# Optimization experiments

Measured on AMD Instinct MI355X. Metric: run time of the kernel, lower is better.

## Reference

```python
import jax, jax.numpy as jnp
import numpy as np

N_EMBED = 1024
HEAD_SIZE = 64
SEQ_LEN = 4096
BATCH = 4


def setup_inputs() -> dict:
    key = jax.random.key(0)
    ks = jax.random.split(key, 7)
    scale = 1.0 / np.sqrt(N_EMBED)
    return {
        "x": jax.random.normal(ks[0], (BATCH, SEQ_LEN, N_EMBED), dtype=jnp.float32),
        "Wq": jax.random.normal(ks[1], (N_EMBED, HEAD_SIZE), dtype=jnp.float32) * scale,
        "bq": jax.random.normal(ks[2], (HEAD_SIZE,), dtype=jnp.float32) * 0.01,
        "Wk": jax.random.normal(ks[3], (N_EMBED, HEAD_SIZE), dtype=jnp.float32) * scale,
        "bk": jax.random.normal(ks[4], (HEAD_SIZE,), dtype=jnp.float32) * 0.01,
        "Wv": jax.random.normal(ks[5], (N_EMBED, HEAD_SIZE), dtype=jnp.float32) * scale,
        "bv": jax.random.normal(ks[6], (HEAD_SIZE,), dtype=jnp.float32) * 0.01,
    }


def reference(x, Wq, bq, Wk, bk, Wv, bv):
    # q, k, v: [B, S, H]
    q = x @ Wq + bq
    k = x @ Wk + bk
    v = x @ Wv + bv
    # raw scores [B, S, S]; original masks to -inf THEN divides by sqrt(head_size)
    # (-inf / sqrt = -inf, so equivalent to scaling finite entries only)
    scores = jnp.einsum("bqh,bkh->bqk", q, k)
    seq_len = x.shape[1]
    causal = jnp.tril(jnp.ones((seq_len, seq_len), dtype=bool))
    inv_scale = 1.0 / jnp.sqrt(jnp.asarray(HEAD_SIZE, dtype=scores.dtype))
    scores = jnp.where(causal, scores * inv_scale, -jnp.inf)
    weight = jax.nn.softmax(scores, axis=-1)
    # dropout is identity in eval / p=0
    out = jnp.einsum("bqk,bkh->bqh", weight, v)
    return out
```

## Files before the change

kernel.cpp:

```cpp
#include <hip/hip_runtime.h>
#include <hip/hip_bf16.h>

#define SS 4096
#define NROW 16384

typedef __attribute__((ext_vector_type(8))) short short8;
typedef __attribute__((ext_vector_type(4))) float f32x4;
typedef _Float16 half4 __attribute__((ext_vector_type(4)));

#define AS1 __attribute__((address_space(1)))
#define AS3 __attribute__((address_space(3)))

static __device__ __forceinline__ void glds16(const void* g, void* l) {
    __builtin_amdgcn_global_load_lds((const AS1 unsigned*)g, (AS3 unsigned*)l, 16, 0, 0);
}
static __device__ __forceinline__ short f2bf(float f) {
    union { float f; unsigned u; } v; v.f = f;
    unsigned r = v.u + 0x7FFFu + ((v.u >> 16) & 1u);
    return (short)(r >> 16);
}
static __device__ __forceinline__ unsigned pkbf(float lo, float hi) {
    union { float f; unsigned u; } x, y; x.f = lo; y.f = hi;
    return __builtin_amdgcn_perm(y.u + 0x8000u, x.u + 0x8000u, 0x07060302);
}
static __device__ __forceinline__ float bf2f(short s) {
    union { unsigned u; float f; } v;
    v.u = ((unsigned)(unsigned short)s) << 16;
    return v.f;
}

__global__ __launch_bounds__(256) void pack_w(const float* __restrict__ Wq,
                                              const float* __restrict__ Wk,
                                              const float* __restrict__ Wv,
                                              short* __restrict__ Wpack) {
    __shared__ float T[64 * 65];
    int bid = blockIdx.x;
    int nb = bid >> 4, kb = bid & 15;
    const float* W = (nb == 0) ? Wq : (nb == 1 ? Wk : Wv);
    int n0 = nb * 64, k0 = kb * 64;
    int tid = threadIdx.x;
    for (int ps = 0; ps < 16; ++ps) {
        int idx = tid + ps * 256;
        int kk = idx >> 6, nn = idx & 63;
        T[kk * 65 + nn] = W[(k0 + kk) * 64 + nn];
    }
    __syncthreads();
    for (int ps = 0; ps < 16; ++ps) {
        int idx = tid + ps * 256;
        int nn = idx >> 6, kk = idx & 63;
        Wpack[(n0 + nn) * 1024 + k0 + kk] = f2bf(T[kk * 65 + nn]);
    }
}

__global__ __launch_bounds__(256, 2) void proj_qkv(const float* __restrict__ x,
                                                   const short* __restrict__ Wpack,
                                                   const float* __restrict__ bq,
                                                   const float* __restrict__ bk,
                                                   const float* __restrict__ bv,
                                                   short* __restrict__ Qg,
                                                   short* __restrict__ Kg,
                                                   short* __restrict__ Vt) {
    __shared__ float Xs[2][32 * 64];
    __shared__ short Wsm[2][192 * 64];
    int tid = threadIdx.x, lane = tid & 63, wv = tid >> 6;
    int g = lane >> 4, c = lane & 15;
    int mh = wv & 1, nh = wv >> 1;
    int rowbase = blockIdx.x * 32;

    f32x4 acc[6];
    for (int i = 0; i < 6; ++i) acc[i] = (f32x4)(0.f);

    int xs0 = (wv * 2 + 0) * 64 + lane, xs1 = (wv * 2 + 1) * 64 + lane;
    int xr0 = xs0 >> 4, xp0 = (xs0 & 15) ^ (xr0 & 15);
    int xr1 = xs1 >> 4, xp1 = (xs1 & 15) ^ (xr1 & 15);

#define PROJ_ISSUE(nbs, k0)                                                              \
    do {                                                                                 \
        glds16(x + (rowbase + xr0) * 1024 + (k0) + xp0 * 4, &Xs[nbs][(wv * 2 + 0) * 256]); \
        glds16(x + (rowbase + xr1) * 1024 + (k0) + xp1 * 4, &Xs[nbs][(wv * 2 + 1) * 256]); \
        for (int j = 0; j < 6; ++j) {                                                    \
            int ws = (wv * 6 + j) * 64 + lane;                                           \
            int wr = ws >> 3, wp = (ws & 7) ^ (wr & 7);                                  \
            glds16(Wpack + wr * 1024 + (k0) + wp * 8, &Wsm[nbs][(wv * 6 + j) * 512]);    \
        }                                                                                \
    } while (0)

    PROJ_ISSUE(0, 0);

    for (int ko = 0; ko < 16; ++ko) {
        int bs = ko & 1;
        __syncthreads();
        if (ko < 15) PROJ_ISSUE(bs ^ 1, (ko + 1) * 64);
        for (int kc = 0; kc < 2; ++kc) {
            int h0 = kc * 8 + g * 2;
            float4 xa = *reinterpret_cast<const float4*>(&Xs[bs][(mh * 16 + c) * 64 + ((h0) ^ c) * 4]);
            float4 xb = *reinterpret_cast<const float4*>(&Xs[bs][(mh * 16 + c) * 64 + ((h0 + 1) ^ c) * 4]);
            short8 a;
            unsigned* aw = (unsigned*)&a;
            aw[0] = pkbf(xa.x, xa.y); aw[1] = pkbf(xa.z, xa.w);
            aw[2] = pkbf(xb.x, xb.y); aw[3] = pkbf(xb.z, xb.w);
            for (int nt = 0; nt < 6; ++nt) {
                int wrow = nh * 96 + nt * 16 + c;
                short8 b = *reinterpret_cast<const short8*>(&Wsm[bs][wrow * 64 + ((g + 4 * kc) ^ (c & 7)) * 8]);
                acc[nt] = __builtin_amdgcn_mfma_f32_16x16x32_bf16(a, b, acc[nt], 0, 0, 0);
            }
        }
    }
#undef PROJ_ISSUE

    const float SCQ = 0.125f * 1.4426950408889634f;
    _Float16* Vh = (_Float16*)Vt;
    for (int nt = 0; nt < 6; ++nt) {
        int col = nh * 96 + nt * 16 + c;
        for (int r = 0; r < 4; ++r) {
            int grow = rowbase + mh * 16 + g * 4 + r;
            float vv = acc[nt][r];
            if (col < 64) {
                Qg[grow * 64 + col] = f2bf((vv + bq[col]) * SCQ);
            } else if (col < 128) {
                Kg[grow * 64 + (col - 64)] = f2bf(vv + bk[col - 64]);
            } else {
                int f = col - 128;
                int batch = grow >> 12, s = grow & 4095;
                int key = s & 63;
                Vh[batch * 262144 + (s >> 6) * 4096 + f * 64 + (key ^ ((f & 15) * 4))] =
                    (_Float16)(vv + bv[f]);
            }
        }
    }
}

__global__ __launch_bounds__(256, 4) void attn(const short* __restrict__ Qg,
                                               const short* __restrict__ Kg,
                                               const short* __restrict__ Vt,
                                               short* __restrict__ Opart,
                                               float* __restrict__ Ls) {
    __shared__ short Kbuf[2][64 * 64];
    __shared__ short Vbuf[2][64 * 64];
    int tid = threadIdx.x, lane = tid & 63, wv = tid >> 6;
    int g = lane >> 4, c = lane & 15;

    int rb = 1151 - blockIdx.x;
    int batch = rb / 288;
    int j = rb - batch * 288;
    int gq = (int)((sqrtf((float)j + 1.0f) - 1.0f) * 0.5f);
    while (4 * (gq + 1) * (gq + 2) <= j) ++gq;
    while (4 * gq * (gq + 1) > j) --gq;
    int rem = j - 4 * gq * (gq + 1);
    int pidx = rem / (gq + 1);
    int ch = rem - pidx * (gq + 1);
    int p = gq * 8 + pidx;

    int t0 = ch * 8, t1 = min(t0 + 8, p + 1);
    int qrow0 = batch * SS + p * 64;
    const short* Kb = Kg + batch * SS * 64;
    const short* Vb = Vt + batch * SS * 64;

    short8 aq0 = *reinterpret_cast<const short8*>(Qg + (qrow0 + wv * 16 + c) * 64 + g * 8);
    short8 aq1 = *reinterpret_cast<const short8*>(Qg + (qrow0 + wv * 16 + c) * 64 + 32 + g * 8);

    f32x4 acc_o[4];
    for (int f = 0; f < 4; ++f) acc_o[f] = (f32x4)(0.f);
    float rs = 0.f;

    int s0 = wv * 128 + lane, s1 = s0 + 64;
    int r0 = s0 >> 3, q0 = (s0 & 7) ^ (r0 & 7);
    int r1 = s1 >> 3, q1 = (s1 & 7) ^ (r1 & 7);

#define ATTN_ISSUE(nbs, t)                                                  \
    do {                                                                    \
        glds16(Kb + (t) * 4096 + r0 * 64 + q0 * 8, &Kbuf[nbs][s0 * 8]);     \
        glds16(Kb + (t) * 4096 + r1 * 64 + q1 * 8, &Kbuf[nbs][s1 * 8]);     \
        glds16(Vb + (t) * 4096 + s0 * 8, &Vbuf[nbs][s0 * 8]);               \
        glds16(Vb + (t) * 4096 + s1 * 8, &Vbuf[nbs][s1 * 8]);               \
    } while (0)

    ATTN_ISSUE(0, t0);

    for (int t = t0; t < t1; ++t) {
        int bs = (t - t0) & 1;
        __syncthreads();
        if (t + 1 < t1) ATTN_ISSUE(bs ^ 1, t + 1);

        f32x4 s[4];
#pragma unroll
        for (int nt = 0; nt < 4; ++nt) {
            short8 k0 = *reinterpret_cast<const short8*>(&Kbuf[bs][(nt * 16 + c) * 64 + ((g) ^ (c & 7)) * 8]);
            short8 k1 = *reinterpret_cast<const short8*>(&Kbuf[bs][(nt * 16 + c) * 64 + ((g + 4) ^ (c & 7)) * 8]);
            s[nt] = (f32x4)(0.f);
            s[nt] = __builtin_amdgcn_mfma_f32_16x16x32_bf16(k0, aq0, s[nt], 0, 0, 0);
            s[nt] = __builtin_amdgcn_mfma_f32_16x16x32_bf16(k1, aq1, s[nt], 0, 0, 0);
        }

        half4 pb[4];
        if (t == p) {
#pragma unroll
            for (int nt = 0; nt < 4; ++nt)
                for (int r = 0; r < 4; ++r) {
                    int key = nt * 16 + g * 4 + r;
                    int row = wv * 16 + c;
                    float pv = (key <= row) ? __builtin_amdgcn_exp2f(s[nt][r]) : 0.f;
                    rs += pv;
                    pb[nt][r] = (_Float16)pv;
                }
        } else {
#pragma unroll
            for (int nt = 0; nt < 4; ++nt)
                for (int r = 0; r < 4; ++r) {
                    float pv = __builtin_amdgcn_exp2f(s[nt][r]);
                    rs += pv;
                    pb[nt][r] = (_Float16)pv;
                }
        }

#pragma unroll
        for (int nt = 0; nt < 4; ++nt) {
#pragma unroll
            for (int ft = 0; ft < 4; ++ft) {
                half4 va = *reinterpret_cast<const half4*>(
                    &Vbuf[bs][(ft * 16 + c) * 64 + ((nt * 16 + g * 4) ^ (c * 4))]);
                acc_o[ft] = __builtin_amdgcn_mfma_f32_16x16x16f16(va, pb[nt], acc_o[ft], 0, 0, 0);
            }
        }
    }
#undef ATTN_ISSUE

    float l = rs;
    l += __shfl_xor(l, 16);
    l += __shfl_xor(l, 32);
    float inv = 1.0f / l;

    int slot = ((batch * 64 + p) << 3) + ch;
    short* op = Opart + slot * 4096;
    int row = wv * 16 + c;
#pragma unroll
    for (int ft = 0; ft < 4; ++ft) {
        short4 ov;
        ov.x = f2bf(acc_o[ft][0] * inv);
        ov.y = f2bf(acc_o[ft][1] * inv);
        ov.z = f2bf(acc_o[ft][2] * inv);
        ov.w = f2bf(acc_o[ft][3] * inv);
        *reinterpret_cast<short4*>(op + row * 64 + ft * 16 + g * 4) = ov;
    }
    if (g == 0)
        Ls[slot * 64 + wv * 16 + c] = l;
}

__global__ __launch_bounds__(256) void merge_k(const short* __restrict__ Opart,
                                               const float* __restrict__ Ls,
                                               float* __restrict__ out) {
    int bP = blockIdx.x;
    int P = bP & 63, batch = bP >> 6;
    int nch = (P + 8) >> 3;
    int tid = threadIdx.x;
    int row = tid & 63, fg = tid >> 6;
    int slot0 = bP << 3;

    float w[8];
    float wsum = 0.f;
    for (int i = 0; i < nch; ++i) { w[i] = Ls[(slot0 + i) * 64 + row]; wsum += w[i]; }
    float invw = 1.0f / wsum;

    float o[16];
    for (int jj = 0; jj < 16; ++jj) o[jj] = 0.f;
    for (int i = 0; i < nch; ++i) {
        const short* op = Opart + (slot0 + i) * 4096 + row * 64 + fg * 16;
        short8 v0 = *reinterpret_cast<const short8*>(op);
        short8 v1 = *reinterpret_cast<const short8*>(op + 8);
        for (int jj = 0; jj < 8; ++jj) {
            o[jj]     += w[i] * bf2f(v0[jj]);
            o[8 + jj] += w[i] * bf2f(v1[jj]);
        }
    }
    int orow = batch * SS + P * 64 + row;
    for (int jj = 0; jj < 16; jj += 4) {
        float4 v;
        v.x = o[jj] * invw; v.y = o[jj + 1] * invw; v.z = o[jj + 2] * invw; v.w = o[jj + 3] * invw;
        *reinterpret_cast<float4*>(out + orow * 64 + fg * 16 + jj) = v;
    }
}

extern "C" void kernel_launch(void* const* d_in, const int* in_sizes, int n_in,
                              void* d_out, int out_size, void* d_ws, size_t ws_size,
                              hipStream_t stream) {
    const float* x  = (const float*)d_in[0];
    const float* Wq = (const float*)d_in[1];
    const float* bq = (const float*)d_in[2];
    const float* Wk = (const float*)d_in[3];
    const float* bk = (const float*)d_in[4];
    const float* Wv = (const float*)d_in[5];
    const float* bv = (const float*)d_in[6];
    float* out = (float*)d_out;

    short* Wpack = (short*)d_ws;
    short* Qg    = Wpack + 196608;
    short* Kg    = Qg + NROW * 64;
    short* Vt    = Kg + NROW * 64;
    short* Opart = Vt + NROW * 64;
    float* Ls    = (float*)(Opart + 2048 * 4096);

    hipLaunchKernelGGL(pack_w,   dim3(48),   dim3(256), 0, stream, Wq, Wk, Wv, Wpack);
    hipLaunchKernelGGL(proj_qkv, dim3(512),  dim3(256), 0, stream, x, Wpack, bq, bk, bv, Qg, Kg, Vt);
    hipLaunchKernelGGL(attn,     dim3(1152), dim3(256), 0, stream, Qg, Kg, Vt, Opart, Ls);
    hipLaunchKernelGGL(merge_k,  dim3(256),  dim3(256), 0, stream, Opart, Ls, out);
}
```

Baseline: 152.1 us.

## Shrink projection tiles to 16 rows and K=32 for more blocks in flight

The QKV projection kernel now has each block handle 16 rows instead of 32 and stages 32-wide K chunks instead of 64. The grid doubles to 1024 blocks and launch bounds allow 4 blocks per CU, with smaller LDS buffers and accumulators and reworked swizzles for the new tile shapes. The goal is better occupancy and more parallelism in this memory-bound pass over x. In exchange, the W tile is reloaded twice as often per row and there are twice as many barrier iterations.

```diff
diff --git a/kernel.cpp b/kernel.cpp
--- a/kernel.cpp
+++ b/kernel.cpp
@@ -52,7 +52,7 @@
     }
 }
 
-__global__ __launch_bounds__(256, 2) void proj_qkv(const float* __restrict__ x,
+__global__ __launch_bounds__(256, 4) void proj_qkv(const float* __restrict__ x,
                                                    const short* __restrict__ Wpack,
                                                    const float* __restrict__ bq,
                                                    const float* __restrict__ bk,
@@ -60,60 +60,57 @@
                                                    short* __restrict__ Qg,
                                                    short* __restrict__ Kg,
                                                    short* __restrict__ Vt) {
-    __shared__ float Xs[2][32 * 64];
-    __shared__ short Wsm[2][192 * 64];
+    __shared__ float Xs[2][16 * 32];
+    __shared__ short Wsm[2][192 * 32];
     int tid = threadIdx.x, lane = tid & 63, wv = tid >> 6;
     int g = lane >> 4, c = lane & 15;
-    int mh = wv & 1, nh = wv >> 1;
-    int rowbase = blockIdx.x * 32;
-
-    f32x4 acc[6];
-    for (int i = 0; i < 6; ++i) acc[i] = (f32x4)(0.f);
-
-    int xs0 = (wv * 2 + 0) * 64 + lane, xs1 = (wv * 2 + 1) * 64 + lane;
-    int xr0 = xs0 >> 4, xp0 = (xs0 & 15) ^ (xr0 & 15);
-    int xr1 = xs1 >> 4, xp1 = (xs1 & 15) ^ (xr1 & 15);
-
-#define PROJ_ISSUE(nbs, k0)                                                              \
-    do {                                                                                 \
-        glds16(x + (rowbase + xr0) * 1024 + (k0) + xp0 * 4, &Xs[nbs][(wv * 2 + 0) * 256]); \
-        glds16(x + (rowbase + xr1) * 1024 + (k0) + xp1 * 4, &Xs[nbs][(wv * 2 + 1) * 256]); \
-        for (int j = 0; j < 6; ++j) {                                                    \
-            int ws = (wv * 6 + j) * 64 + lane;                                           \
-            int wr = ws >> 3, wp = (ws & 7) ^ (wr & 7);                                  \
-            glds16(Wpack + wr * 1024 + (k0) + wp * 8, &Wsm[nbs][(wv * 6 + j) * 512]);    \
-        }                                                                                \
+    int rowbase = blockIdx.x * 16;
+
+    f32x4 acc[3];
+    for (int i = 0; i < 3; ++i) acc[i] = (f32x4)(0.f);
+
+    int xrow = tid >> 3, xq = tid & 7;
+    int xsrc = xq ^ (xrow & 7);
+
+#define PROJ_ISSUE(nbs, k0)                                                               \
+    do {                                                                                  \
+        if (tid < 128)                                                                    \
+            glds16(x + (rowbase + xrow) * 1024 + (k0) + xsrc * 4, &Xs[nbs][tid * 4]);     \
+        for (int j = 0; j < 3; ++j) {                                                     \
+            int u = (wv * 3 + j) * 64 + lane;                                             \
+            int wr = u >> 2, wq = u & 3;                                                  \
+            glds16(Wpack + wr * 1024 + (k0) + (wq ^ ((wr >> 1) & 3)) * 8,                 \
+                   &Wsm[nbs][u * 8]);                                                     \
+        }                                                                                 \
     } while (0)
 
     PROJ_ISSUE(0, 0);
 
-    for (int ko = 0; ko < 16; ++ko) {
+    for (int ko = 0; ko < 32; ++ko) {
         int bs = ko & 1;
         __syncthreads();
-        if (ko < 15) PROJ_ISSUE(bs ^ 1, (ko + 1) * 64);
-        for (int kc = 0; kc < 2; ++kc) {
-            int h0 = kc * 8 + g * 2;
-            float4 xa = *reinterpret_cast<const float4*>(&Xs[bs][(mh * 16 + c) * 64 + ((h0) ^ c) * 4]);
-            float4 xb = *reinterpret_cast<const float4*>(&Xs[bs][(mh * 16 + c) * 64 + ((h0 + 1) ^ c) * 4]);
-            short8 a;
-            unsigned* aw = (unsigned*)&a;
-            aw[0] = pkbf(xa.x, xa.y); aw[1] = pkbf(xa.z, xa.w);
-            aw[2] = pkbf(xb.x, xb.y); aw[3] = pkbf(xb.z, xb.w);
-            for (int nt = 0; nt < 6; ++nt) {
-                int wrow = nh * 96 + nt * 16 + c;
-                short8 b = *reinterpret_cast<const short8*>(&Wsm[bs][wrow * 64 + ((g + 4 * kc) ^ (c & 7)) * 8]);
-                acc[nt] = __builtin_amdgcn_mfma_f32_16x16x32_bf16(a, b, acc[nt], 0, 0, 0);
-            }
+        if (ko < 31) PROJ_ISSUE(bs ^ 1, (ko + 1) * 32);
+        float4 xa = *reinterpret_cast<const float4*>(&Xs[bs][c * 32 + ((2 * g) ^ (c & 7)) * 4]);
+        float4 xb = *reinterpret_cast<const float4*>(&Xs[bs][c * 32 + ((2 * g + 1) ^ (c & 7)) * 4]);
+        short8 a;
+        unsigned* aw = (unsigned*)&a;
+        aw[0] = pkbf(xa.x, xa.y); aw[1] = pkbf(xa.z, xa.w);
+        aw[2] = pkbf(xb.x, xb.y); aw[3] = pkbf(xb.z, xb.w);
+        for (int nt = 0; nt < 3; ++nt) {
+            int wrow = wv * 48 + nt * 16 + c;
+            short8 b = *reinterpret_cast<const short8*>(
+                &Wsm[bs][wrow * 32 + (g ^ ((wrow >> 1) & 3)) * 8]);
+            acc[nt] = __builtin_amdgcn_mfma_f32_16x16x32_bf16(a, b, acc[nt], 0, 0, 0);
         }
     }
 #undef PROJ_ISSUE
 
     const float SCQ = 0.125f * 1.4426950408889634f;
     _Float16* Vh = (_Float16*)Vt;
-    for (int nt = 0; nt < 6; ++nt) {
-        int col = nh * 96 + nt * 16 + c;
+    for (int nt = 0; nt < 3; ++nt) {
+        int col = wv * 48 + nt * 16 + c;
         for (int r = 0; r < 4; ++r) {
-            int grow = rowbase + mh * 16 + g * 4 + r;
+            int grow = rowbase + g * 4 + r;
             float vv = acc[nt][r];
             if (col < 64) {
                 Qg[grow * 64 + col] = f2bf((vv + bq[col]) * SCQ);
@@ -300,7 +297,7 @@
     float* Ls    = (float*)(Opart + 2048 * 4096);
 
     hipLaunchKernelGGL(pack_w,   dim3(48),   dim3(256), 0, stream, Wq, Wk, Wv, Wpack);
-    hipLaunchKernelGGL(proj_qkv, dim3(512),  dim3(256), 0, stream, x, Wpack, bq, bk, bv, Qg, Kg, Vt);
+    hipLaunchKernelGGL(proj_qkv, dim3(1024), dim3(256), 0, stream, x, Wpack, bq, bk, bv, Qg, Kg, Vt);
     hipLaunchKernelGGL(attn,     dim3(1152), dim3(256), 0, stream, Qg, Kg, Vt, Opart, Ls);
     hipLaunchKernelGGL(merge_k,  dim3(256),  dim3(256), 0, stream, Opart, Ls, out);
 }
```

After: 169.2 us. 1.11x slower.
